# Kernel tuning notes

Measured on AMD Instinct MI355X. Metric: run time of the kernel, lower is better.

The kernel has to match this reference:

```python
import jax, jax.numpy as jnp
import numpy as np

B, T, D_MODEL = 2, 2048, 2048
N_HEAD, N_KV = 16, 4
HEAD_DIM = D_MODEL // N_HEAD  # 128
N_REP = N_HEAD // N_KV        # 4
ROPE_BASE = 10000.0


def setup_inputs() -> dict:
    key = jax.random.key(0)
    ks = jax.random.split(key, 5)
    s = 0.02
    return {
        "x": jax.random.normal(ks[0], (B, T, D_MODEL), dtype=jnp.float32),
        "Wq": jax.random.normal(ks[1], (D_MODEL, N_HEAD * HEAD_DIM), dtype=jnp.float32) * s,
        "Wk": jax.random.normal(ks[2], (D_MODEL, N_KV * HEAD_DIM), dtype=jnp.float32) * s,
        "Wv": jax.random.normal(ks[3], (D_MODEL, N_KV * HEAD_DIM), dtype=jnp.float32) * s,
        "Wo": jax.random.normal(ks[4], (D_MODEL, D_MODEL), dtype=jnp.float32) * s,
    }


def _rope_cos_sin(seq_len, dim, dtype):
    inv_freq = 1.0 / (ROPE_BASE ** (jnp.arange(0, dim, 2, dtype=jnp.float32) / dim))
    t = jnp.arange(seq_len, dtype=jnp.float32)
    freqs = t[:, None] * inv_freq[None, :]          # (T, dim/2)
    emb = jnp.concatenate([freqs, freqs], axis=-1)  # (T, dim)
    return jnp.cos(emb).astype(dtype), jnp.sin(emb).astype(dtype)


def _rotate_half(x):
    half = x.shape[-1] // 2
    return jnp.concatenate([-x[..., half:], x[..., :half]], axis=-1)


def reference(x, Wq, Wk, Wv, Wo):
    Bx, Tx, _ = x.shape
    # projections (weights stored (in, out); equals torch Linear with W^T)
    q = (x @ Wq).reshape(Bx, Tx, N_HEAD, HEAD_DIM).transpose(0, 2, 1, 3)  # (B,H,T,d)
    k = (x @ Wk).reshape(Bx, Tx, N_KV, HEAD_DIM).transpose(0, 2, 1, 3)    # (B,Hkv,T,d)
    v = (x @ Wv).reshape(Bx, Tx, N_KV, HEAD_DIM).transpose(0, 2, 1, 3)

    cos, sin = _rope_cos_sin(Tx, HEAD_DIM, x.dtype)  # (T, d)
    q = q * cos + _rotate_half(q) * sin
    k = k * cos + _rotate_half(k) * sin

    # grouped attention: q grouped by kv head, avoids materializing repeated K/V
    qg = q.reshape(Bx, N_KV, N_REP, Tx, HEAD_DIM)
    scale = 1.0 / np.sqrt(HEAD_DIM)
    att = jnp.einsum('bgrtd,bgsd->bgrts', qg, k) * scale  # (B,Hkv,rep,T,S)
    causal = jnp.tril(jnp.ones((Tx, Tx), dtype=bool))
    att = jnp.where(causal, att, -jnp.inf)
    att = jax.nn.softmax(att, axis=-1)
    y = jnp.einsum('bgrts,bgsd->bgrtd', att, v)           # (B,Hkv,rep,T,d)
    y = y.reshape(Bx, N_HEAD, Tx, HEAD_DIM).transpose(0, 2, 1, 3).reshape(Bx, Tx, D_MODEL)
    return y @ Wo
```

## Files before the change

### kernel.cpp

```cpp
#include <hip/hip_runtime.h>
#include <hip/hip_bf16.h>

typedef unsigned short u16;
typedef unsigned int u32;
typedef __attribute__((ext_vector_type(4))) float f32x4;
typedef __attribute__((ext_vector_type(8))) __bf16 bf16x8;

#define B_   2
#define T_   2048
#define DM   2048
#define NH   16
#define NKV  4
#define HD   128

__device__ __forceinline__ u16 f2bf(float f){
    u32 u = __builtin_bit_cast(u32, f);
    u += 0x7FFFu + ((u >> 16) & 1u);
    return (u16)(u >> 16);
}
__device__ __forceinline__ float bf2f(u16 v){
    return __builtin_bit_cast(float, (u32)v << 16);
}

__device__ __forceinline__ float ex2(float x){
    float r; asm("v_exp_f32 %0, %1" : "=v"(r) : "v"(x)); return r;
}

__device__ __forceinline__ void gld_lds16(const void* g, void* l){
    __builtin_amdgcn_global_load_lds(
        (const __attribute__((address_space(1))) void*)g,
        (__attribute__((address_space(3))) void*)l, 16, 0, 0);
}

__global__ void prep(const float* __restrict__ x,
                     const float* __restrict__ Wq, const float* __restrict__ Wk,
                     const float* __restrict__ Wv, const float* __restrict__ Wo,
                     u16* __restrict__ xb, u16* __restrict__ Wqkv, u16* __restrict__ Wot,
                     float2* __restrict__ tab){
    __shared__ float tile[32][33];
    int bid = blockIdx.x, tid = threadIdx.x;
    if (bid < 8192){
        int i = bid * 256 + tid;
        float4 v = ((const float4*)x)[i];
        ushort4 o;
        o.x = f2bf(v.x); o.y = f2bf(v.y); o.z = f2bf(v.z); o.w = f2bf(v.w);
        ((ushort4*)xb)[i] = o;
    } else if (bid < 18432){
        int tb = bid - 8192;
        int bx = tb % 160, byy = tb / 160;
        const float* W; u16* Out; int N; int nb; int perm;
        if (bx < 64)      { W = Wq; Out = Wqkv;                  N = 2048; nb = bx;      perm = 1; }
        else if (bx < 80) { W = Wk; Out = Wqkv + 2048ull * 2048; N = 512;  nb = bx - 64; perm = 1; }
        else if (bx < 96) { W = Wv; Out = Wqkv + 2560ull * 2048; N = 512;  nb = bx - 80; perm = 0; }
        else              { W = Wo; Out = Wot;                   N = 2048; nb = bx - 96; perm = 0; }
        int n0 = nb * 32, k0 = byy * 32;
        int tx = tid & 31, ty = tid >> 5;
#pragma unroll
        for (int i = 0; i < 4; i++)
            tile[ty + i * 8][tx] = W[(size_t)(k0 + ty + i * 8) * N + n0 + tx];
        __syncthreads();
#pragma unroll
        for (int i = 0; i < 4; i++){
            int n = n0 + ty + i * 8;
            int np = perm ? ((n & ~127) | ((n & 63) << 1) | ((n >> 6) & 1)) : n;
            Out[(size_t)np * 2048 + k0 + tx] = f2bf(tile[tx][ty + i * 8]);
        }
    } else {
        int idx = (bid - 18432) * 256 + tid;
        int i = idx & 63, t = idx >> 6;
        float ang = (float)t * exp2f((float)i * (-13.287712379549449f / 64.0f));
        float sv, cv;
        __sincosf(ang, &sv, &cv);
        tab[idx] = make_float2(cv, sv);
    }
}

#define BARR() asm volatile("s_barrier" ::: "memory")
#define VM4()  asm volatile("s_waitcnt vmcnt(4)" ::: "memory")
#define VM8()  asm volatile("s_waitcnt vmcnt(8)" ::: "memory")

#define READ_A(QA, BUF) { \
    const char* ab = (const char*)&As[BUF][wm][0]; \
    _Pragma("unroll") for (int i = 0; i < 4; i++){ \
        int rh = ((QA)*4 + i)*16 + lx; \
        _Pragma("unroll") for (int ks = 0; ks < 2; ks++) \
            a_[i][ks] = *(const bf16x8*)(ab + rh*128 + (((ks*4+tg)*16) ^ ((lx&7)<<4))); \
    } }
#define READ_B(QB, BUF) { \
    const char* bb = (const char*)&Bs[BUF][wn>>1][0]; \
    _Pragma("unroll") for (int n = 0; n < 2; n++){ \
        int rbh = (wn&1)*64 + ((QB)*2+n)*16 + lx; \
        _Pragma("unroll") for (int ks = 0; ks < 2; ks++) \
            b_[(QB)*2+n][ks] = *(const bf16x8*)(bb + rbh*128 + (((ks*4+tg)*16) ^ ((lx&7)<<4))); \
    } }
#define MFMA_Q(QA, QB) { \
    __builtin_amdgcn_s_setprio(1); \
    _Pragma("unroll") for (int i = 0; i < 4; i++) \
    _Pragma("unroll") for (int n = 0; n < 2; n++) \
    _Pragma("unroll") for (int ks = 0; ks < 2; ks++) \
        acc[(QA)*4+i][(QB)*2+n] = __builtin_amdgcn_mfma_f32_16x16x32_bf16( \
            a_[i][ks], b_[(QB)*2+n][ks], acc[(QA)*4+i][(QB)*2+n], 0, 0, 0); \
    __builtin_amdgcn_s_setprio(0); }

template<int MODE>
__global__ __launch_bounds__(512, 2) void gemm256(const u16* __restrict__ A, const u16* __restrict__ Bt,
                                                  void* __restrict__ O0, u16* __restrict__ Ktl,
                                                  u16* __restrict__ Vtl, const float2* __restrict__ tab,
                                                  int NBX){
    __shared__ __attribute__((aligned(16))) u16 As[2][2][8192];
    __shared__ __attribute__((aligned(16))) u16 Bs[2][2][8192];
    const int tid = threadIdx.x;
    const int lane = tid & 63, w = tid >> 6;
    const int wm = w >> 2, wn = w & 3;
    const int tg = lane >> 4, lx = lane & 15;
    int q8 = (int)gridDim.x >> 3;
    int swz = ((int)blockIdx.x & 7) * q8 + ((int)blockIdx.x >> 3);
    int kh = 0;
    if constexpr (MODE == 2){ kh = swz >> 7; swz &= 127; }
    const int bx = swz % NBX, by = swz / NBX;
    const int m0 = by * 256, n0 = bx * 256;
    const int K = 2048;
    const int NIT = (MODE == 2) ? 8 : 16;
    const int kt0 = kh * 16;
    const int ltMax = 2 * NIT - 1;
    const int kcx = (lane & 7) ^ ((lane >> 3) & 7);

    f32x4 acc[8][4];
    const f32x4 Z = {0.f, 0.f, 0.f, 0.f};
#pragma unroll
    for (int i = 0; i < 8; i++)
#pragma unroll
        for (int j = 0; j < 4; j++) acc[i][j] = Z;
    bf16x8 a_[4][2], b_[4][2];

    auto stA = [&](int buf, int q, int kt){
        int mh = w >> 2;
        int s0 = (w & 3) * 2;
#pragma unroll
        for (int l = 0; l < 2; l++){
            int s = s0 + l;
            gld_lds16(A + (size_t)(m0 + mh*128 + q*64 + s*8 + (lane>>3)) * K + kt*64 + kcx*8,
                      &As[buf][mh][q*4096 + s*512 + lane*8]);
        }
    };
    auto stB = [&](int buf, int q, int kt){
        int bh = w >> 2;
        int hi = (w >> 1) & 1;
        int s0 = (w & 1) * 2;
#pragma unroll
        for (int l = 0; l < 2; l++){
            int s = s0 + l;
            gld_lds16(Bt + (size_t)(n0 + bh*128 + hi*64 + q*32 + s*8 + (lane>>3)) * K + kt*64 + kcx*8,
                      &Bs[buf][bh][hi*4096 + q*2048 + s*512 + lane*8]);
        }
    };

    stA(0, 0, kt0); stB(0, 0, kt0); stA(0, 1, kt0); stB(0, 1, kt0);
    stA(1, 0, kt0 + 1); stB(1, 0, kt0 + 1);
    VM4(); BARR();

#pragma unroll 1
    for (int it = 0; it < NIT; it++){
        const int T1 = kt0 + 2*it + 1;
        const int T2 = kt0 + ((2*it + 2 < ltMax) ? 2*it + 2 : ltMax);
        const int T3 = kt0 + ((2*it + 3 < ltMax) ? 2*it + 3 : ltMax);
        READ_A(0, 0); READ_B(0, 0); stA(1, 1, T1);
        BARR(); MFMA_Q(0, 0); BARR();
        READ_B(1, 0); stB(1, 1, T1);
        BARR(); MFMA_Q(0, 1); BARR();
        READ_A(1, 0); stA(0, 0, T2);
        BARR(); MFMA_Q(1, 0); BARR();
        stB(0, 0, T2);
        BARR(); MFMA_Q(1, 1); VM4(); BARR();
        READ_A(0, 1); READ_B(0, 1); stA(0, 1, T2);
        BARR(); MFMA_Q(0, 0); BARR();
        READ_B(1, 1); stB(0, 1, T2);
        BARR(); MFMA_Q(0, 1); BARR();
        READ_A(1, 1); stA(1, 0, T3);
        BARR(); MFMA_Q(1, 0); BARR();
        stB(1, 0, T3);
        BARR(); MFMA_Q(1, 1); VM4(); BARR();
    }

    if constexpr (MODE == 2){
        u16* C = (u16*)O0 + (size_t)kh * 4096 * 2048;
#pragma unroll
        for (int mi = 0; mi < 8; mi++)
#pragma unroll
            for (int ni = 0; ni < 4; ni++){
                int r0 = m0 + wm*128 + mi*16 + tg*4;
                int c  = n0 + wn*64 + ni*16 + lx;
#pragma unroll
                for (int j = 0; j < 4; j++)
                    C[(size_t)(r0 + j) * 2048 + c] = f2bf(acc[mi][ni][j]);
            }
    } else {
        u16* Qp = (u16*)O0;
        if (bx < 8){
            const float QS = 0.08838834764831845f * 1.4426950408889634f;
#pragma unroll
            for (int mi = 0; mi < 8; mi++)
#pragma unroll
                for (int ni = 0; ni < 4; ni++){
                    int r0 = m0 + wm*128 + mi*16 + tg*4;
                    int c  = n0 + wn*64 + ni*16 + lx;
                    int ii = (c & 127) >> 1;
#pragma unroll
                    for (int j = 0; j < 4; j++){
                        float v = acc[mi][ni][j];
                        float p = __shfl_xor(v, 1);
                        int t = (r0 + j) & 2047;
                        float2 cs = tab[t * 64 + ii];
                        float o = ((lx & 1) ? (v * cs.x + p * cs.y) : (v * cs.x - p * cs.y)) * QS;
                        Qp[(size_t)(r0 + j) * 2048 + c] = f2bf(o);
                    }
                }
        } else if (bx < 10){
#pragma unroll
            for (int mi = 0; mi < 8; mi++)
#pragma unroll
                for (int ni = 0; ni < 4; ni++){
                    int r0 = m0 + wm*128 + mi*16 + tg*4;
                    int c  = n0 + wn*64 + ni*16 + lx;
                    int hk = (c >> 7) & 3;
                    int dd = c & 127;
                    int ii = dd >> 1;
#pragma unroll
                    for (int j = 0; j < 4; j++){
                        int r = r0 + j;
                        int bb2 = r >> 11, tt = r & 2047;
                        float v = acc[mi][ni][j];
                        float p = __shfl_xor(v, 1);
                        float2 cs = tab[tt * 64 + ii];
                        float o = (lx & 1) ? (v * cs.x + p * cs.y) : (v * cs.x - p * cs.y);
                        size_t tb = ((size_t)(bb2 * 4 + hk) * 32 + (tt >> 6)) * 8192;
                        u32 byte = (u32)((tt & 63) * 256) + (((u32)(2 * dd)) ^ ((u32)((tt & 7) << 4)));
                        Ktl[tb + byte / 2] = f2bf(o);
                    }
                }
        } else {
#pragma unroll
            for (int mi = 0; mi < 8; mi++){
                int r0 = m0 + wm*128 + mi*16 + tg*4;
                int bb2 = r0 >> 11, ss = r0 & 2047;
                int sb = ss & 63;
#pragma unroll
                for (int ni = 0; ni < 4; ni++){
                    int c  = n0 + wn*64 + ni*16 + lx;
                    int hk = (c >> 7) & 3;
                    int d  = c & 127;
                    size_t tb = ((size_t)(bb2 * 4 + hk) * 32 + (ss >> 6)) * 8192;
                    u32 swzd = (u32)((d & 7) << 4);
#pragma unroll
                    for (int j = 0; j < 4; j++){
                        int s = sb + j;
                        int sig = ((s & 15) << 2) | ((s >> 4) & 3);
                        u32 byte = (u32)(d * 128) + (((u32)(2 * sig)) ^ swzd);
                        Vtl[tb + byte / 2] = f2bf(acc[mi][ni][j]);
                    }
                }
            }
        }
    }
}

__global__ void reduceWo(const u16* __restrict__ P, float* __restrict__ out){
    size_t t = (size_t)blockIdx.x * 256 + threadIdx.x;
    const u16* p0 = P + t * 8;
    const u16* p1 = P + 4096ull * 2048 + t * 8;
    uint4 a = *(const uint4*)p0;
    uint4 b = *(const uint4*)p1;
    const u16* as = (const u16*)&a;
    const u16* bs = (const u16*)&b;
    float4 o0, o1;
    o0.x = bf2f(as[0]) + bf2f(bs[0]); o0.y = bf2f(as[1]) + bf2f(bs[1]);
    o0.z = bf2f(as[2]) + bf2f(bs[2]); o0.w = bf2f(as[3]) + bf2f(bs[3]);
    o1.x = bf2f(as[4]) + bf2f(bs[4]); o1.y = bf2f(as[5]) + bf2f(bs[5]);
    o1.z = bf2f(as[6]) + bf2f(bs[6]); o1.w = bf2f(as[7]) + bf2f(bs[7]);
    ((float4*)out)[t * 2]     = o0;
    ((float4*)out)[t * 2 + 1] = o1;
}

__global__ __launch_bounds__(256) void attn5(const u16* __restrict__ Q, const u16* __restrict__ Kt,
                                             const u16* __restrict__ Vt, u16* __restrict__ Y){
    __shared__ __attribute__((aligned(16))) u16 Ks[2][64 * 128];
    __shared__ __attribute__((aligned(16))) u16 Vs[2][64 * 128];
    __shared__ __attribute__((aligned(16))) u16 Pl[4][16 * 64];
    const int lane = threadIdx.x & 63, w = threadIdx.x >> 6;
    const int jb = blockIdx.x, h = blockIdx.y, b = blockIdx.z;
    const int hkv = h >> 2;
    const size_t kvBase = ((size_t)(b * NKV + hkv) * 32) * 8192;
    const f32x4 Z = {0.f, 0.f, 0.f, 0.f};
    const int tg = lane >> 4, lx = lane & 15;

    auto STAGE = [&](int buf, int it){
        const u16* kg = Kt + kvBase + (size_t)it * 8192;
        const u16* vg = Vt + kvBase + (size_t)it * 8192;
#pragma unroll
        for (int i = 0; i < 4; i++){
            int is = w * 4 + i;
            gld_lds16(kg + is * 512 + lane * 8, &Ks[buf][is * 512]);
            gld_lds16(vg + is * 512 + lane * 8, &Vs[buf][is * 512]);
        }
    };

#pragma unroll 1
    for (int pass = 0; pass < 2; pass++){
        const int qt = pass == 0 ? jb : 31 - jb;
        const int q0 = qt * 64;
        const int qrow = q0 + w * 16 + lx;
        bf16x8 qfr[4];
#pragma unroll
        for (int kk = 0; kk < 4; kk++)
            qfr[kk] = *(const bf16x8*)(Q + (size_t)(b * T_ + qrow) * DM + h * HD + kk * 32 + tg * 8);
        f32x4 accO[8];
#pragma unroll
        for (int i = 0; i < 8; i++) accO[i] = Z;
        float mr[4] = {-INFINITY, -INFINITY, -INFINITY, -INFINITY};
        float lp[4] = {0.f, 0.f, 0.f, 0.f};
        const int nIter = qt + 1;

        STAGE(0, 0);
        __syncthreads();
        int cur = 0;

#pragma unroll 1
        for (int it = 0; it < nIter; it++){
            if (it + 1 < nIter) STAGE(cur ^ 1, it + 1);
            f32x4 sa[4];
#pragma unroll
            for (int c = 0; c < 4; c++) sa[c] = Z;
            __builtin_amdgcn_s_setprio(1);
#pragma unroll
            for (int c = 0; c < 4; c++){
                int s = c * 16 + lx;
                u32 swz = (u32)((s & 7) << 4);
                const char* kb = (const char*)&Ks[cur][0] + s * 256;
#pragma unroll
                for (int kk = 0; kk < 4; kk++){
                    bf16x8 kf = *(const bf16x8*)(kb + (((u32)(kk * 64 + tg * 16)) ^ swz));
                    sa[c] = __builtin_amdgcn_mfma_f32_16x16x32_bf16(qfr[kk], kf, sa[c], 0, 0, 0);
                }
            }
            __builtin_amdgcn_s_setprio(0);
            const bool diag = (it == nIter - 1);
            float tl[4];
#pragma unroll
            for (int j = 0; j < 4; j++){
                float a0 = sa[0][j], a1 = sa[1][j], a2 = sa[2][j], a3 = sa[3][j];
                if (diag){
                    int qloc = w * 16 + tg * 4 + j;
                    if (lx      > qloc) a0 = -INFINITY;
                    if (lx + 16 > qloc) a1 = -INFINITY;
                    if (lx + 32 > qloc) a2 = -INFINITY;
                    if (lx + 48 > qloc) a3 = -INFINITY;
                }
                sa[0][j] = a0; sa[1][j] = a1; sa[2][j] = a2; sa[3][j] = a3;
                tl[j] = fmaxf(fmaxf(a0, a1), fmaxf(a2, a3));
            }
            int lok = (tl[0] <= mr[0] + 8.f) && (tl[1] <= mr[1] + 8.f) &&
                      (tl[2] <= mr[2] + 8.f) && (tl[3] <= mr[3] + 8.f);
            if (!__all(lok)){
                float corr[4];
#pragma unroll
                for (int j = 0; j < 4; j++){
                    float t = tl[j];
                    t = fmaxf(t, __shfl_xor(t, 1));
                    t = fmaxf(t, __shfl_xor(t, 2));
                    t = fmaxf(t, __shfl_xor(t, 4));
                    t = fmaxf(t, __shfl_xor(t, 8));
                    float mn = fmaxf(mr[j], t);
                    corr[j] = ex2(mr[j] - mn);
                    mr[j] = mn;
                    lp[j] *= corr[j];
                }
#pragma unroll
                for (int dt = 0; dt < 8; dt++){
                    f32x4 t = accO[dt];
                    t[0] *= corr[0]; t[1] *= corr[1]; t[2] *= corr[2]; t[3] *= corr[3];
                    accO[dt] = t;
                }
            }
#pragma unroll
            for (int j = 0; j < 4; j++){
                float mn = mr[j];
                float p0 = ex2(sa[0][j] - mn), p1 = ex2(sa[1][j] - mn);
                float p2 = ex2(sa[2][j] - mn), p3 = ex2(sa[3][j] - mn);
                lp[j] += p0 + p1 + p2 + p3;
                int rr = tg * 4 + j;
                u32 woff = (u32)(rr * 128) + (((u32)(lx * 8)) ^ ((u32)((rr & 7) << 4)));
                u32 r01, r23;
                asm("v_cvt_pk_bf16_f32 %0, %1, %2" : "=v"(r01) : "v"(p0), "v"(p1));
                asm("v_cvt_pk_bf16_f32 %0, %1, %2" : "=v"(r23) : "v"(p2), "v"(p3));
                uint2 pk2 = make_uint2(r01, r23);
                *(uint2*)((char*)&Pl[w][0] + woff) = pk2;
            }
            bf16x8 pf[2];
            {
                char* pb = (char*)&Pl[w][0] + lx * 128;
                u32 swz = (u32)((lx & 7) << 4);
                pf[0] = *(const bf16x8*)(pb + (((u32)(tg * 16))      ^ swz));
                pf[1] = *(const bf16x8*)(pb + (((u32)(tg * 16 + 64)) ^ swz));
            }
            __builtin_amdgcn_s_setprio(1);
#pragma unroll
            for (int dt = 0; dt < 8; dt++){
                int d = dt * 16 + lx;
                u32 swz = (u32)((d & 7) << 4);
                const char* vb = (const char*)&Vs[cur][0] + d * 128;
                bf16x8 vf0 = *(const bf16x8*)(vb + (((u32)(tg * 16))      ^ swz));
                bf16x8 vf1 = *(const bf16x8*)(vb + (((u32)(tg * 16 + 64)) ^ swz));
                accO[dt] = __builtin_amdgcn_mfma_f32_16x16x32_bf16(pf[0], vf0, accO[dt], 0, 0, 0);
                accO[dt] = __builtin_amdgcn_mfma_f32_16x16x32_bf16(pf[1], vf1, accO[dt], 0, 0, 0);
            }
            __builtin_amdgcn_s_setprio(0);
            __syncthreads();
            cur ^= 1;
        }
        float inv[4];
#pragma unroll
        for (int j = 0; j < 4; j++){
            float s = lp[j];
            s += __shfl_xor(s, 1);
            s += __shfl_xor(s, 2);
            s += __shfl_xor(s, 4);
            s += __shfl_xor(s, 8);
            inv[j] = 1.0f / s;
        }
#pragma unroll
        for (int dt = 0; dt < 8; dt++)
#pragma unroll
            for (int j = 0; j < 4; j++){
                int qr = q0 + w * 16 + tg * 4 + j;
                int d = dt * 16 + lx;
                Y[(size_t)(b * T_ + qr) * DM + h * HD + d] = f2bf(accO[dt][j] * inv[j]);
            }
    }
}

extern "C" void kernel_launch(void* const* d_in, const int* in_sizes, int n_in,
                              void* d_out, int out_size, void* d_ws, size_t ws_size,
                              hipStream_t stream){
    const float* x  = (const float*)d_in[0];
    const float* Wq = (const float*)d_in[1];
    const float* Wk = (const float*)d_in[2];
    const float* Wv = (const float*)d_in[3];
    const float* Wo = (const float*)d_in[4];

    char* ws = (char*)d_ws;
    size_t off = 0;
    auto alloc = [&](size_t bytes){ void* p = ws + off; off += (bytes + 255) & ~255ull; return p; };
    u16*    xb   = (u16*)alloc(4096ull * 2048 * 2);
    u16*    Wqkv = (u16*)alloc(3072ull * 2048 * 2);
    u16*    Wot  = (u16*)alloc(2048ull * 2048 * 2);
    u16*    qbb  = (u16*)alloc(4096ull * 2048 * 2);
    u16*    ktl  = (u16*)alloc(2ull * 4 * 32 * 8192 * 2);
    u16*    vtl  = (u16*)alloc(2ull * 4 * 32 * 8192 * 2);
    u16*    ybb  = (u16*)alloc(4096ull * 2048 * 2);
    u16*    pbb  = (u16*)alloc(2ull * 4096 * 2048 * 2);
    float2* tab  = (float2*)alloc(2048ull * 64 * 8);

    prep<<<18944, 256, 0, stream>>>(x, Wq, Wk, Wv, Wo, xb, Wqkv, Wot, tab);

    gemm256<1><<<192, 512, 0, stream>>>(xb, Wqkv, qbb, ktl, vtl, tab, 12);

    attn5<<<dim3(16, 16, 2), 256, 0, stream>>>(qbb, ktl, vtl, ybb);

    gemm256<2><<<256, 512, 0, stream>>>(ybb, Wot, pbb, nullptr, nullptr, nullptr, 8);
    reduceWo<<<4096, 256, 0, stream>>>(pbb, (float*)d_out);
}
```

Baseline: 203.5 us.

## Split attention into single-tile blocks with 32-key tiles and deepen GEMM prefetch

The attention kernel now launches one block per 64-row query tile, 1024 blocks in total, instead of one block looping over two paired tiles. An interleaved block ordering balances the causal workload across blocks. K/V tiles shrink from 64 to 32 keys, and the V layout written by the QKV GEMM epilogue is changed to match, which lowers LDS use and register pressure and should raise occupancy. The price is more loop iterations and barriers per block. The GEMM main loop also issues the whole next k-tile earlier and waits with vmcnt(8), aiming to hide more global-load latency.

New measurement: 225.9 us. +11.0%, slower.

```diff
diff --git a/kernel.cpp b/kernel.cpp
--- a/kernel.cpp
+++ b/kernel.cpp
@@ -76,7 +76,6 @@
 }
 
 #define BARR() asm volatile("s_barrier" ::: "memory")
-#define VM4()  asm volatile("s_waitcnt vmcnt(4)" ::: "memory")
 #define VM8()  asm volatile("s_waitcnt vmcnt(8)" ::: "memory")
 
 #define READ_A(QA, BUF) { \
@@ -156,30 +155,29 @@
     };
 
     stA(0, 0, kt0); stB(0, 0, kt0); stA(0, 1, kt0); stB(0, 1, kt0);
-    stA(1, 0, kt0 + 1); stB(1, 0, kt0 + 1);
-    VM4(); BARR();
+    stA(1, 0, kt0 + 1); stB(1, 0, kt0 + 1); stB(1, 1, kt0 + 1); stA(1, 1, kt0 + 1);
+    VM8(); BARR();
 
 #pragma unroll 1
     for (int it = 0; it < NIT; it++){
-        const int T1 = kt0 + 2*it + 1;
         const int T2 = kt0 + ((2*it + 2 < ltMax) ? 2*it + 2 : ltMax);
         const int T3 = kt0 + ((2*it + 3 < ltMax) ? 2*it + 3 : ltMax);
-        READ_A(0, 0); READ_B(0, 0); stA(1, 1, T1);
+        READ_A(0, 0); READ_B(0, 0);
         BARR(); MFMA_Q(0, 0); BARR();
-        READ_B(1, 0); stB(1, 1, T1);
+        READ_B(1, 0); stA(0, 0, T2); stB(0, 0, T2);
         BARR(); MFMA_Q(0, 1); BARR();
-        READ_A(1, 0); stA(0, 0, T2);
+        READ_A(1, 0); stB(0, 1, T2);
         BARR(); MFMA_Q(1, 0); BARR();
-        stB(0, 0, T2);
-        BARR(); MFMA_Q(1, 1); VM4(); BARR();
-        READ_A(0, 1); READ_B(0, 1); stA(0, 1, T2);
+        stA(0, 1, T2);
+        BARR(); MFMA_Q(1, 1); VM8(); BARR();
+        READ_A(0, 1); READ_B(0, 1);
         BARR(); MFMA_Q(0, 0); BARR();
-        READ_B(1, 1); stB(0, 1, T2);
+        READ_B(1, 1); stA(1, 0, T3); stB(1, 0, T3);
         BARR(); MFMA_Q(0, 1); BARR();
-        READ_A(1, 1); stA(1, 0, T3);
+        READ_A(1, 1); stB(1, 1, T3);
         BARR(); MFMA_Q(1, 0); BARR();
-        stB(1, 0, T3);
-        BARR(); MFMA_Q(1, 1); VM4(); BARR();
+        stA(1, 1, T3);
+        BARR(); MFMA_Q(1, 1); VM8(); BARR();
     }
 
     if constexpr (MODE == 2){
@@ -243,20 +241,20 @@
             for (int mi = 0; mi < 8; mi++){
                 int r0 = m0 + wm*128 + mi*16 + tg*4;
                 int bb2 = r0 >> 11, ss = r0 & 2047;
-                int sb = ss & 63;
+                int sb = ss & 31;
 #pragma unroll
                 for (int ni = 0; ni < 4; ni++){
                     int c  = n0 + wn*64 + ni*16 + lx;
                     int hk = (c >> 7) & 3;
                     int d  = c & 127;
-                    size_t tb = ((size_t)(bb2 * 4 + hk) * 32 + (ss >> 6)) * 8192;
-                    u32 swzd = (u32)((d & 7) << 4);
+                    size_t tbh = ((size_t)(bb2 * 4 + hk) * 64 + (ss >> 5)) * 4096;
+                    u32 swzd = (u32)((d & 3) << 4);
 #pragma unroll
                     for (int j = 0; j < 4; j++){
                         int s = sb + j;
-                        int sig = ((s & 15) << 2) | ((s >> 4) & 3);
-                        u32 byte = (u32)(d * 128) + (((u32)(2 * sig)) ^ swzd);
-                        Vtl[tb + byte / 2] = f2bf(acc[mi][ni][j]);
+                        int sig = ((s & 15) << 1) | ((s >> 4) & 1);
+                        u32 byte = (u32)(d * 64) + (((u32)(2 * sig)) ^ swzd);
+                        Vtl[tbh + byte / 2] = f2bf(acc[mi][ni][j]);
                     }
                 }
             }
@@ -281,161 +279,149 @@
     ((float4*)out)[t * 2 + 1] = o1;
 }
 
-__global__ __launch_bounds__(256) void attn5(const u16* __restrict__ Q, const u16* __restrict__ Kt,
+__global__ __launch_bounds__(256) void attn7(const u16* __restrict__ Q, const u16* __restrict__ Kt,
                                              const u16* __restrict__ Vt, u16* __restrict__ Y){
-    __shared__ __attribute__((aligned(16))) u16 Ks[2][64 * 128];
-    __shared__ __attribute__((aligned(16))) u16 Vs[2][64 * 128];
-    __shared__ __attribute__((aligned(16))) u16 Pl[4][16 * 64];
-    const int lane = threadIdx.x & 63, w = threadIdx.x >> 6;
-    const int jb = blockIdx.x, h = blockIdx.y, b = blockIdx.z;
+    __shared__ __attribute__((aligned(16))) u16 Ks[2][4096];
+    __shared__ __attribute__((aligned(16))) u16 Vs[2][4096];
+    __shared__ __attribute__((aligned(16))) u16 Pl[4][512];
+    const int tid = threadIdx.x;
+    const int lane = tid & 63, w = tid >> 6;
+    const int tg = lane >> 4, lx = lane & 15;
+    int gid = blockIdx.x;
+    int z = gid & 255, k4 = gid >> 8;
+    int j8 = z & 7, h = (z >> 3) & 15, b = z >> 7;
+    int qt = (k4 == 0) ? j8 : (k4 == 1) ? 31 - j8 : (k4 == 2) ? j8 + 8 : 23 - j8;
     const int hkv = h >> 2;
-    const size_t kvBase = ((size_t)(b * NKV + hkv) * 32) * 8192;
+    const size_t kvBase = (size_t)(b * NKV + hkv) * 64 * 4096;
     const f32x4 Z = {0.f, 0.f, 0.f, 0.f};
-    const int tg = lane >> 4, lx = lane & 15;
 
     auto STAGE = [&](int buf, int it){
-        const u16* kg = Kt + kvBase + (size_t)it * 8192;
-        const u16* vg = Vt + kvBase + (size_t)it * 8192;
-#pragma unroll
-        for (int i = 0; i < 4; i++){
-            int is = w * 4 + i;
-            gld_lds16(kg + is * 512 + lane * 8, &Ks[buf][is * 512]);
-            gld_lds16(vg + is * 512 + lane * 8, &Vs[buf][is * 512]);
-        }
+        const u16* kg = Kt + kvBase + (size_t)it * 4096;
+        const u16* vg = Vt + kvBase + (size_t)it * 4096;
+        gld_lds16(kg + tid * 8,        &Ks[buf][tid * 8]);
+        gld_lds16(kg + 2048 + tid * 8, &Ks[buf][2048 + tid * 8]);
+        gld_lds16(vg + tid * 8,        &Vs[buf][tid * 8]);
+        gld_lds16(vg + 2048 + tid * 8, &Vs[buf][2048 + tid * 8]);
     };
 
+    const int q0 = qt * 64;
+    const int qrow = q0 + w * 16 + lx;
+    bf16x8 qfr[4];
+#pragma unroll
+    for (int kk = 0; kk < 4; kk++)
+        qfr[kk] = *(const bf16x8*)(Q + (size_t)(b * T_ + qrow) * DM + h * HD + kk * 32 + tg * 8);
+    f32x4 accO[8];
+#pragma unroll
+    for (int i = 0; i < 8; i++) accO[i] = Z;
+    float mr[4] = {-INFINITY, -INFINITY, -INFINITY, -INFINITY};
+    float lp[4] = {0.f, 0.f, 0.f, 0.f};
+    const int nIter = 2 * qt + 2;
+
+    STAGE(0, 0);
+    __syncthreads();
+    int cur = 0;
+
 #pragma unroll 1
-    for (int pass = 0; pass < 2; pass++){
-        const int qt = pass == 0 ? jb : 31 - jb;
-        const int q0 = qt * 64;
-        const int qrow = q0 + w * 16 + lx;
-        bf16x8 qfr[4];
-#pragma unroll
-        for (int kk = 0; kk < 4; kk++)
-            qfr[kk] = *(const bf16x8*)(Q + (size_t)(b * T_ + qrow) * DM + h * HD + kk * 32 + tg * 8);
-        f32x4 accO[8];
-#pragma unroll
-        for (int i = 0; i < 8; i++) accO[i] = Z;
-        float mr[4] = {-INFINITY, -INFINITY, -INFINITY, -INFINITY};
-        float lp[4] = {0.f, 0.f, 0.f, 0.f};
-        const int nIter = qt + 1;
-
-        STAGE(0, 0);
+    for (int it = 0; it < nIter; it++){
+        if (it + 1 < nIter) STAGE(cur ^ 1, it + 1);
+        f32x4 sa[2];
+        sa[0] = Z; sa[1] = Z;
+        __builtin_amdgcn_s_setprio(1);
+#pragma unroll
+        for (int c = 0; c < 2; c++){
+            int s = c * 16 + lx;
+            u32 swz = (u32)((s & 7) << 4);
+            const char* kb = (const char*)&Ks[cur][0] + s * 256;
+#pragma unroll
+            for (int kk = 0; kk < 4; kk++){
+                bf16x8 kf = *(const bf16x8*)(kb + (((u32)(kk * 64 + tg * 16)) ^ swz));
+                sa[c] = __builtin_amdgcn_mfma_f32_16x16x32_bf16(qfr[kk], kf, sa[c], 0, 0, 0);
+            }
+        }
+        __builtin_amdgcn_s_setprio(0);
+        const int s0g = it * 32;
+        const bool diag = (s0g + 31 > q0 + w * 16);
+        float tl[4];
+#pragma unroll
+        for (int j = 0; j < 4; j++){
+            float a0 = sa[0][j], a1 = sa[1][j];
+            if (diag){
+                int qg = q0 + w * 16 + tg * 4 + j;
+                if (s0g + lx > qg)      a0 = -INFINITY;
+                if (s0g + 16 + lx > qg) a1 = -INFINITY;
+            }
+            sa[0][j] = a0; sa[1][j] = a1;
+            tl[j] = fmaxf(a0, a1);
+        }
+        int lok = (tl[0] <= mr[0] + 8.f) && (tl[1] <= mr[1] + 8.f) &&
+                  (tl[2] <= mr[2] + 8.f) && (tl[3] <= mr[3] + 8.f);
+        if (!__all(lok)){
+            float corr[4];
+#pragma unroll
+            for (int j = 0; j < 4; j++){
+                float t = tl[j];
+                t = fmaxf(t, __shfl_xor(t, 1));
+                t = fmaxf(t, __shfl_xor(t, 2));
+                t = fmaxf(t, __shfl_xor(t, 4));
+                t = fmaxf(t, __shfl_xor(t, 8));
+                float mn = fmaxf(mr[j], t);
+                corr[j] = ex2(mr[j] - mn);
+                mr[j] = mn;
+                lp[j] *= corr[j];
+            }
+#pragma unroll
+            for (int dt = 0; dt < 8; dt++){
+                f32x4 t = accO[dt];
+                t[0] *= corr[0]; t[1] *= corr[1]; t[2] *= corr[2]; t[3] *= corr[3];
+                accO[dt] = t;
+            }
+        }
+#pragma unroll
+        for (int j = 0; j < 4; j++){
+            float mn = mr[j];
+            float p0 = ex2(sa[0][j] - mn), p1 = ex2(sa[1][j] - mn);
+            lp[j] += p0 + p1;
+            int rr = tg * 4 + j;
+            u32 woff = (u32)(rr * 64) + (((u32)(lx * 4)) ^ ((u32)((rr & 3) << 4)));
+            u32 r01;
+            asm("v_cvt_pk_bf16_f32 %0, %1, %2" : "=v"(r01) : "v"(p0), "v"(p1));
+            *(u32*)((char*)&Pl[w][0] + woff) = r01;
+        }
+        bf16x8 pf;
+        {
+            char* pb = (char*)&Pl[w][0] + lx * 64;
+            pf = *(const bf16x8*)(pb + (((u32)(tg * 16)) ^ ((u32)((lx & 3) << 4))));
+        }
+        __builtin_amdgcn_s_setprio(1);
+#pragma unroll
+        for (int dt = 0; dt < 8; dt++){
+            int d = dt * 16 + lx;
+            const char* vb = (const char*)&Vs[cur][0] + d * 64;
+            bf16x8 vf = *(const bf16x8*)(vb + (((u32)(tg * 16)) ^ ((u32)((d & 3) << 4))));
+            accO[dt] = __builtin_amdgcn_mfma_f32_16x16x32_bf16(pf, vf, accO[dt], 0, 0, 0);
+        }
+        __builtin_amdgcn_s_setprio(0);
         __syncthreads();
-        int cur = 0;
-
-#pragma unroll 1
-        for (int it = 0; it < nIter; it++){
-            if (it + 1 < nIter) STAGE(cur ^ 1, it + 1);
-            f32x4 sa[4];
-#pragma unroll
-            for (int c = 0; c < 4; c++) sa[c] = Z;
-            __builtin_amdgcn_s_setprio(1);
-#pragma unroll
-            for (int c = 0; c < 4; c++){
-                int s = c * 16 + lx;
-                u32 swz = (u32)((s & 7) << 4);
-                const char* kb = (const char*)&Ks[cur][0] + s * 256;
-#pragma unroll
-                for (int kk = 0; kk < 4; kk++){
-                    bf16x8 kf = *(const bf16x8*)(kb + (((u32)(kk * 64 + tg * 16)) ^ swz));
-                    sa[c] = __builtin_amdgcn_mfma_f32_16x16x32_bf16(qfr[kk], kf, sa[c], 0, 0, 0);
-                }
-            }
-            __builtin_amdgcn_s_setprio(0);
-            const bool diag = (it == nIter - 1);
-            float tl[4];
-#pragma unroll
-            for (int j = 0; j < 4; j++){
-                float a0 = sa[0][j], a1 = sa[1][j], a2 = sa[2][j], a3 = sa[3][j];
-                if (diag){
-                    int qloc = w * 16 + tg * 4 + j;
-                    if (lx      > qloc) a0 = -INFINITY;
-                    if (lx + 16 > qloc) a1 = -INFINITY;
-                    if (lx + 32 > qloc) a2 = -INFINITY;
-                    if (lx + 48 > qloc) a3 = -INFINITY;
-                }
-                sa[0][j] = a0; sa[1][j] = a1; sa[2][j] = a2; sa[3][j] = a3;
-                tl[j] = fmaxf(fmaxf(a0, a1), fmaxf(a2, a3));
-            }
-            int lok = (tl[0] <= mr[0] + 8.f) && (tl[1] <= mr[1] + 8.f) &&
-                      (tl[2] <= mr[2] + 8.f) && (tl[3] <= mr[3] + 8.f);
-            if (!__all(lok)){
-                float corr[4];
-#pragma unroll
-                for (int j = 0; j < 4; j++){
-                    float t = tl[j];
-                    t = fmaxf(t, __shfl_xor(t, 1));
-                    t = fmaxf(t, __shfl_xor(t, 2));
-                    t = fmaxf(t, __shfl_xor(t, 4));
-                    t = fmaxf(t, __shfl_xor(t, 8));
-                    float mn = fmaxf(mr[j], t);
-                    corr[j] = ex2(mr[j] - mn);
-                    mr[j] = mn;
-                    lp[j] *= corr[j];
-                }
-#pragma unroll
-                for (int dt = 0; dt < 8; dt++){
-                    f32x4 t = accO[dt];
-                    t[0] *= corr[0]; t[1] *= corr[1]; t[2] *= corr[2]; t[3] *= corr[3];
-                    accO[dt] = t;
-                }
-            }
-#pragma unroll
-            for (int j = 0; j < 4; j++){
-                float mn = mr[j];
-                float p0 = ex2(sa[0][j] - mn), p1 = ex2(sa[1][j] - mn);
-                float p2 = ex2(sa[2][j] - mn), p3 = ex2(sa[3][j] - mn);
-                lp[j] += p0 + p1 + p2 + p3;
-                int rr = tg * 4 + j;
-                u32 woff = (u32)(rr * 128) + (((u32)(lx * 8)) ^ ((u32)((rr & 7) << 4)));
-                u32 r01, r23;
-                asm("v_cvt_pk_bf16_f32 %0, %1, %2" : "=v"(r01) : "v"(p0), "v"(p1));
-                asm("v_cvt_pk_bf16_f32 %0, %1, %2" : "=v"(r23) : "v"(p2), "v"(p3));
-                uint2 pk2 = make_uint2(r01, r23);
-                *(uint2*)((char*)&Pl[w][0] + woff) = pk2;
-            }
-            bf16x8 pf[2];
-            {
-                char* pb = (char*)&Pl[w][0] + lx * 128;
-                u32 swz = (u32)((lx & 7) << 4);
-                pf[0] = *(const bf16x8*)(pb + (((u32)(tg * 16))      ^ swz));
-                pf[1] = *(const bf16x8*)(pb + (((u32)(tg * 16 + 64)) ^ swz));
-            }
-            __builtin_amdgcn_s_setprio(1);
-#pragma unroll
-            for (int dt = 0; dt < 8; dt++){
-                int d = dt * 16 + lx;
-                u32 swz = (u32)((d & 7) << 4);
-                const char* vb = (const char*)&Vs[cur][0] + d * 128;
-                bf16x8 vf0 = *(const bf16x8*)(vb + (((u32)(tg * 16))      ^ swz));
-                bf16x8 vf1 = *(const bf16x8*)(vb + (((u32)(tg * 16 + 64)) ^ swz));
-                accO[dt] = __builtin_amdgcn_mfma_f32_16x16x32_bf16(pf[0], vf0, accO[dt], 0, 0, 0);
-                accO[dt] = __builtin_amdgcn_mfma_f32_16x16x32_bf16(pf[1], vf1, accO[dt], 0, 0, 0);
-            }
-            __builtin_amdgcn_s_setprio(0);
-            __syncthreads();
-            cur ^= 1;
-        }
-        float inv[4];
+        cur ^= 1;
+    }
+    float inv[4];
+#pragma unroll
+    for (int j = 0; j < 4; j++){
+        float s = lp[j];
+        s += __shfl_xor(s, 1);
+        s += __shfl_xor(s, 2);
+        s += __shfl_xor(s, 4);
+        s += __shfl_xor(s, 8);
+        inv[j] = 1.0f / s;
+    }
+#pragma unroll
+    for (int dt = 0; dt < 8; dt++)
 #pragma unroll
         for (int j = 0; j < 4; j++){
-            float s = lp[j];
-            s += __shfl_xor(s, 1);
-            s += __shfl_xor(s, 2);
-            s += __shfl_xor(s, 4);
-            s += __shfl_xor(s, 8);
-            inv[j] = 1.0f / s;
-        }
-#pragma unroll
-        for (int dt = 0; dt < 8; dt++)
-#pragma unroll
-            for (int j = 0; j < 4; j++){
-                int qr = q0 + w * 16 + tg * 4 + j;
-                int d = dt * 16 + lx;
-                Y[(size_t)(b * T_ + qr) * DM + h * HD + d] = f2bf(accO[dt][j] * inv[j]);
-            }
-    }
+            int qr = q0 + w * 16 + tg * 4 + j;
+            int d = dt * 16 + lx;
+            Y[(size_t)(b * T_ + qr) * DM + h * HD + d] = f2bf(accO[dt][j] * inv[j]);
+        }
 }
 
 extern "C" void kernel_launch(void* const* d_in, const int* in_sizes, int n_in,
@@ -454,8 +440,8 @@
     u16*    Wqkv = (u16*)alloc(3072ull * 2048 * 2);
     u16*    Wot  = (u16*)alloc(2048ull * 2048 * 2);
     u16*    qbb  = (u16*)alloc(4096ull * 2048 * 2);
-    u16*    ktl  = (u16*)alloc(2ull * 4 * 32 * 8192 * 2);
-    u16*    vtl  = (u16*)alloc(2ull * 4 * 32 * 8192 * 2);
+    u16*    ktl  = (u16*)alloc(2ull * 4 * 64 * 4096 * 2);
+    u16*    vtl  = (u16*)alloc(2ull * 4 * 64 * 4096 * 2);
     u16*    ybb  = (u16*)alloc(4096ull * 2048 * 2);
     u16*    pbb  = (u16*)alloc(2ull * 4096 * 2048 * 2);
     float2* tab  = (float2*)alloc(2048ull * 64 * 8);
@@ -464,7 +450,7 @@
 
     gemm256<1><<<192, 512, 0, stream>>>(xb, Wqkv, qbb, ktl, vtl, tab, 12);
 
-    attn5<<<dim3(16, 16, 2), 256, 0, stream>>>(qbb, ktl, vtl, ybb);
+    attn7<<<1024, 256, 0, stream>>>(qbb, ktl, vtl, ybb);
 
     gemm256<2><<<256, 512, 0, stream>>>(ybb, Wot, pbb, nullptr, nullptr, nullptr, 8);
     reduceWo<<<4096, 256, 0, stream>>>(pbb, (float*)d_out);
```

## Split attention into one q-tile per block with single-buffered K/V staggered prefetch

Applied to the files above, without the earlier changes.

The attention kernel now launches 1024 blocks that each handle one 64-row query tile, where before 512 blocks each ran two causal-balanced passes. Work is ordered so that long and short tiles interleave across the launch. K and V each use a single LDS buffer instead of a double buffer. The next K tile is loaded while softmax and PV run, and the next V tile is loaded after PV, with explicit vmcnt waits and barriers. This halves LDS use so more blocks can be resident and latency is hidden across blocks, at the cost of extra barriers and less prefetch distance within a block.

After: 202.1 us. Within noise of the previous version (-0.7%).

```diff
diff --git a/kernel.cpp b/kernel.cpp
--- a/kernel.cpp
+++ b/kernel.cpp
@@ -76,8 +76,8 @@
 }
 
 #define BARR() asm volatile("s_barrier" ::: "memory")
+#define VM0()  asm volatile("s_waitcnt vmcnt(0)" ::: "memory")
 #define VM4()  asm volatile("s_waitcnt vmcnt(4)" ::: "memory")
-#define VM8()  asm volatile("s_waitcnt vmcnt(8)" ::: "memory")
 
 #define READ_A(QA, BUF) { \
     const char* ab = (const char*)&As[BUF][wm][0]; \
@@ -281,161 +281,170 @@
     ((float4*)out)[t * 2 + 1] = o1;
 }
 
-__global__ __launch_bounds__(256) void attn5(const u16* __restrict__ Q, const u16* __restrict__ Kt,
+__global__ __launch_bounds__(256) void attn8(const u16* __restrict__ Q, const u16* __restrict__ Kt,
                                              const u16* __restrict__ Vt, u16* __restrict__ Y){
-    __shared__ __attribute__((aligned(16))) u16 Ks[2][64 * 128];
-    __shared__ __attribute__((aligned(16))) u16 Vs[2][64 * 128];
-    __shared__ __attribute__((aligned(16))) u16 Pl[4][16 * 64];
-    const int lane = threadIdx.x & 63, w = threadIdx.x >> 6;
-    const int jb = blockIdx.x, h = blockIdx.y, b = blockIdx.z;
+    __shared__ __attribute__((aligned(16))) u16 Ks[8192];
+    __shared__ __attribute__((aligned(16))) u16 Vs[8192];
+    __shared__ __attribute__((aligned(16))) u16 Pl[4][1024];
+    const int tid = threadIdx.x;
+    const int lane = tid & 63, w = tid >> 6;
+    const int tg = lane >> 4, lx = lane & 15;
+    int gid = blockIdx.x;
+    int z = gid & 255, k4 = gid >> 8;
+    int j8 = z & 7, h = (z >> 3) & 15, b = z >> 7;
+    int qt = (k4 == 0) ? j8 : (k4 == 1) ? 31 - j8 : (k4 == 2) ? j8 + 8 : 23 - j8;
     const int hkv = h >> 2;
     const size_t kvBase = ((size_t)(b * NKV + hkv) * 32) * 8192;
     const f32x4 Z = {0.f, 0.f, 0.f, 0.f};
-    const int tg = lane >> 4, lx = lane & 15;
-
-    auto STAGE = [&](int buf, int it){
+
+    auto STAGE_K = [&](int it){
         const u16* kg = Kt + kvBase + (size_t)it * 8192;
-        const u16* vg = Vt + kvBase + (size_t)it * 8192;
 #pragma unroll
         for (int i = 0; i < 4; i++){
             int is = w * 4 + i;
-            gld_lds16(kg + is * 512 + lane * 8, &Ks[buf][is * 512]);
-            gld_lds16(vg + is * 512 + lane * 8, &Vs[buf][is * 512]);
+            gld_lds16(kg + is * 512 + lane * 8, &Ks[is * 512]);
         }
     };
+    auto STAGE_V = [&](int it){
+        const u16* vg = Vt + kvBase + (size_t)it * 8192;
+#pragma unroll
+        for (int i = 0; i < 4; i++){
+            int is = w * 4 + i;
+            gld_lds16(vg + is * 512 + lane * 8, &Vs[is * 512]);
+        }
+    };
+
+    const int q0 = qt * 64;
+    const int qrow = q0 + w * 16 + lx;
+    bf16x8 qfr[4];
+#pragma unroll
+    for (int kk = 0; kk < 4; kk++)
+        qfr[kk] = *(const bf16x8*)(Q + (size_t)(b * T_ + qrow) * DM + h * HD + kk * 32 + tg * 8);
+    f32x4 accO[8];
+#pragma unroll
+    for (int i = 0; i < 8; i++) accO[i] = Z;
+    float mr[4] = {-INFINITY, -INFINITY, -INFINITY, -INFINITY};
+    float lp[4] = {0.f, 0.f, 0.f, 0.f};
+    const int nIter = qt + 1;
+
+    STAGE_K(0); STAGE_V(0);
 
 #pragma unroll 1
-    for (int pass = 0; pass < 2; pass++){
-        const int qt = pass == 0 ? jb : 31 - jb;
-        const int q0 = qt * 64;
-        const int qrow = q0 + w * 16 + lx;
-        bf16x8 qfr[4];
-#pragma unroll
-        for (int kk = 0; kk < 4; kk++)
-            qfr[kk] = *(const bf16x8*)(Q + (size_t)(b * T_ + qrow) * DM + h * HD + kk * 32 + tg * 8);
-        f32x4 accO[8];
-#pragma unroll
-        for (int i = 0; i < 8; i++) accO[i] = Z;
-        float mr[4] = {-INFINITY, -INFINITY, -INFINITY, -INFINITY};
-        float lp[4] = {0.f, 0.f, 0.f, 0.f};
-        const int nIter = qt + 1;
-
-        STAGE(0, 0);
-        __syncthreads();
-        int cur = 0;
-
-#pragma unroll 1
-        for (int it = 0; it < nIter; it++){
-            if (it + 1 < nIter) STAGE(cur ^ 1, it + 1);
-            f32x4 sa[4];
-#pragma unroll
-            for (int c = 0; c < 4; c++) sa[c] = Z;
-            __builtin_amdgcn_s_setprio(1);
-#pragma unroll
-            for (int c = 0; c < 4; c++){
-                int s = c * 16 + lx;
-                u32 swz = (u32)((s & 7) << 4);
-                const char* kb = (const char*)&Ks[cur][0] + s * 256;
-#pragma unroll
-                for (int kk = 0; kk < 4; kk++){
-                    bf16x8 kf = *(const bf16x8*)(kb + (((u32)(kk * 64 + tg * 16)) ^ swz));
-                    sa[c] = __builtin_amdgcn_mfma_f32_16x16x32_bf16(qfr[kk], kf, sa[c], 0, 0, 0);
-                }
-            }
-            __builtin_amdgcn_s_setprio(0);
-            const bool diag = (it == nIter - 1);
-            float tl[4];
+    for (int it = 0; it < nIter; it++){
+        const bool last = (it + 1 == nIter);
+        VM4(); BARR();
+        f32x4 sa[4];
+#pragma unroll
+        for (int c = 0; c < 4; c++) sa[c] = Z;
+        __builtin_amdgcn_s_setprio(1);
+#pragma unroll
+        for (int c = 0; c < 4; c++){
+            int s = c * 16 + lx;
+            u32 swz = (u32)((s & 7) << 4);
+            const char* kb = (const char*)&Ks[0] + s * 256;
+#pragma unroll
+            for (int kk = 0; kk < 4; kk++){
+                bf16x8 kf = *(const bf16x8*)(kb + (((u32)(kk * 64 + tg * 16)) ^ swz));
+                sa[c] = __builtin_amdgcn_mfma_f32_16x16x32_bf16(qfr[kk], kf, sa[c], 0, 0, 0);
+            }
+        }
+        __builtin_amdgcn_s_setprio(0);
+        BARR();
+        if (!last) STAGE_K(it + 1);
+        const bool diag = last;
+        float tl[4];
+#pragma unroll
+        for (int j = 0; j < 4; j++){
+            float a0 = sa[0][j], a1 = sa[1][j], a2 = sa[2][j], a3 = sa[3][j];
+            if (diag){
+                int qloc = w * 16 + tg * 4 + j;
+                if (lx      > qloc) a0 = -INFINITY;
+                if (lx + 16 > qloc) a1 = -INFINITY;
+                if (lx + 32 > qloc) a2 = -INFINITY;
+                if (lx + 48 > qloc) a3 = -INFINITY;
+            }
+            sa[0][j] = a0; sa[1][j] = a1; sa[2][j] = a2; sa[3][j] = a3;
+            tl[j] = fmaxf(fmaxf(a0, a1), fmaxf(a2, a3));
+        }
+        int lok = (tl[0] <= mr[0] + 8.f) && (tl[1] <= mr[1] + 8.f) &&
+                  (tl[2] <= mr[2] + 8.f) && (tl[3] <= mr[3] + 8.f);
+        if (!__all(lok)){
+            float corr[4];
 #pragma unroll
             for (int j = 0; j < 4; j++){
-                float a0 = sa[0][j], a1 = sa[1][j], a2 = sa[2][j], a3 = sa[3][j];
-                if (diag){
-                    int qloc = w * 16 + tg * 4 + j;
-                    if (lx      > qloc) a0 = -INFINITY;
-                    if (lx + 16 > qloc) a1 = -INFINITY;
-                    if (lx + 32 > qloc) a2 = -INFINITY;
-                    if (lx + 48 > qloc) a3 = -INFINITY;
-                }
-                sa[0][j] = a0; sa[1][j] = a1; sa[2][j] = a2; sa[3][j] = a3;
-                tl[j] = fmaxf(fmaxf(a0, a1), fmaxf(a2, a3));
-            }
-            int lok = (tl[0] <= mr[0] + 8.f) && (tl[1] <= mr[1] + 8.f) &&
-                      (tl[2] <= mr[2] + 8.f) && (tl[3] <= mr[3] + 8.f);
-            if (!__all(lok)){
-                float corr[4];
-#pragma unroll
-                for (int j = 0; j < 4; j++){
-                    float t = tl[j];
-                    t = fmaxf(t, __shfl_xor(t, 1));
-                    t = fmaxf(t, __shfl_xor(t, 2));
-                    t = fmaxf(t, __shfl_xor(t, 4));
-                    t = fmaxf(t, __shfl_xor(t, 8));
-                    float mn = fmaxf(mr[j], t);
-                    corr[j] = ex2(mr[j] - mn);
-                    mr[j] = mn;
-                    lp[j] *= corr[j];
-                }
-#pragma unroll
-                for (int dt = 0; dt < 8; dt++){
-                    f32x4 t = accO[dt];
-                    t[0] *= corr[0]; t[1] *= corr[1]; t[2] *= corr[2]; t[3] *= corr[3];
-                    accO[dt] = t;
-                }
-            }
-#pragma unroll
-            for (int j = 0; j < 4; j++){
-                float mn = mr[j];
-                float p0 = ex2(sa[0][j] - mn), p1 = ex2(sa[1][j] - mn);
-                float p2 = ex2(sa[2][j] - mn), p3 = ex2(sa[3][j] - mn);
-                lp[j] += p0 + p1 + p2 + p3;
-                int rr = tg * 4 + j;
-                u32 woff = (u32)(rr * 128) + (((u32)(lx * 8)) ^ ((u32)((rr & 7) << 4)));
-                u32 r01, r23;
-                asm("v_cvt_pk_bf16_f32 %0, %1, %2" : "=v"(r01) : "v"(p0), "v"(p1));
-                asm("v_cvt_pk_bf16_f32 %0, %1, %2" : "=v"(r23) : "v"(p2), "v"(p3));
-                uint2 pk2 = make_uint2(r01, r23);
-                *(uint2*)((char*)&Pl[w][0] + woff) = pk2;
-            }
-            bf16x8 pf[2];
-            {
-                char* pb = (char*)&Pl[w][0] + lx * 128;
-                u32 swz = (u32)((lx & 7) << 4);
-                pf[0] = *(const bf16x8*)(pb + (((u32)(tg * 16))      ^ swz));
-                pf[1] = *(const bf16x8*)(pb + (((u32)(tg * 16 + 64)) ^ swz));
-            }
-            __builtin_amdgcn_s_setprio(1);
+                float t = tl[j];
+                t = fmaxf(t, __shfl_xor(t, 1));
+                t = fmaxf(t, __shfl_xor(t, 2));
+                t = fmaxf(t, __shfl_xor(t, 4));
+                t = fmaxf(t, __shfl_xor(t, 8));
+                float mn = fmaxf(mr[j], t);
+                corr[j] = ex2(mr[j] - mn);
+                mr[j] = mn;
+                lp[j] *= corr[j];
+            }
 #pragma unroll
             for (int dt = 0; dt < 8; dt++){
-                int d = dt * 16 + lx;
-                u32 swz = (u32)((d & 7) << 4);
-                const char* vb = (const char*)&Vs[cur][0] + d * 128;
-                bf16x8 vf0 = *(const bf16x8*)(vb + (((u32)(tg * 16))      ^ swz));
-                bf16x8 vf1 = *(const bf16x8*)(vb + (((u32)(tg * 16 + 64)) ^ swz));
-                accO[dt] = __builtin_amdgcn_mfma_f32_16x16x32_bf16(pf[0], vf0, accO[dt], 0, 0, 0);
-                accO[dt] = __builtin_amdgcn_mfma_f32_16x16x32_bf16(pf[1], vf1, accO[dt], 0, 0, 0);
-            }
-            __builtin_amdgcn_s_setprio(0);
-            __syncthreads();
-            cur ^= 1;
-        }
-        float inv[4];
+                f32x4 t = accO[dt];
+                t[0] *= corr[0]; t[1] *= corr[1]; t[2] *= corr[2]; t[3] *= corr[3];
+                accO[dt] = t;
+            }
+        }
 #pragma unroll
         for (int j = 0; j < 4; j++){
-            float s = lp[j];
-            s += __shfl_xor(s, 1);
-            s += __shfl_xor(s, 2);
-            s += __shfl_xor(s, 4);
-            s += __shfl_xor(s, 8);
-            inv[j] = 1.0f / s;
-        }
-#pragma unroll
-        for (int dt = 0; dt < 8; dt++)
-#pragma unroll
-            for (int j = 0; j < 4; j++){
-                int qr = q0 + w * 16 + tg * 4 + j;
-                int d = dt * 16 + lx;
-                Y[(size_t)(b * T_ + qr) * DM + h * HD + d] = f2bf(accO[dt][j] * inv[j]);
-            }
+            float mn = mr[j];
+            float p0 = ex2(sa[0][j] - mn), p1 = ex2(sa[1][j] - mn);
+            float p2 = ex2(sa[2][j] - mn), p3 = ex2(sa[3][j] - mn);
+            lp[j] += p0 + p1 + p2 + p3;
+            int rr = tg * 4 + j;
+            u32 woff = (u32)(rr * 128) + (((u32)(lx * 8)) ^ ((u32)((rr & 7) << 4)));
+            u32 r01, r23;
+            asm("v_cvt_pk_bf16_f32 %0, %1, %2" : "=v"(r01) : "v"(p0), "v"(p1));
+            asm("v_cvt_pk_bf16_f32 %0, %1, %2" : "=v"(r23) : "v"(p2), "v"(p3));
+            uint2 pk2 = make_uint2(r01, r23);
+            *(uint2*)((char*)&Pl[w][0] + woff) = pk2;
+        }
+        bf16x8 pf[2];
+        {
+            char* pb = (char*)&Pl[w][0] + lx * 128;
+            u32 swz = (u32)((lx & 7) << 4);
+            pf[0] = *(const bf16x8*)(pb + (((u32)(tg * 16))      ^ swz));
+            pf[1] = *(const bf16x8*)(pb + (((u32)(tg * 16 + 64)) ^ swz));
+        }
+        if (last){ VM0(); } else { VM4(); }
+        BARR();
+        __builtin_amdgcn_s_setprio(1);
+#pragma unroll
+        for (int dt = 0; dt < 8; dt++){
+            int d = dt * 16 + lx;
+            u32 swz = (u32)((d & 7) << 4);
+            const char* vb = (const char*)&Vs[0] + d * 128;
+            bf16x8 vf0 = *(const bf16x8*)(vb + (((u32)(tg * 16))      ^ swz));
+            bf16x8 vf1 = *(const bf16x8*)(vb + (((u32)(tg * 16 + 64)) ^ swz));
+            accO[dt] = __builtin_amdgcn_mfma_f32_16x16x32_bf16(pf[0], vf0, accO[dt], 0, 0, 0);
+            accO[dt] = __builtin_amdgcn_mfma_f32_16x16x32_bf16(pf[1], vf1, accO[dt], 0, 0, 0);
+        }
+        __builtin_amdgcn_s_setprio(0);
+        BARR();
+        if (!last) STAGE_V(it + 1);
     }
+    float inv[4];
+#pragma unroll
+    for (int j = 0; j < 4; j++){
+        float s = lp[j];
+        s += __shfl_xor(s, 1);
+        s += __shfl_xor(s, 2);
+        s += __shfl_xor(s, 4);
+        s += __shfl_xor(s, 8);
+        inv[j] = 1.0f / s;
+    }
+#pragma unroll
+    for (int dt = 0; dt < 8; dt++)
+#pragma unroll
+        for (int j = 0; j < 4; j++){
+            int qr = q0 + w * 16 + tg * 4 + j;
+            int d = dt * 16 + lx;
+            Y[(size_t)(b * T_ + qr) * DM + h * HD + d] = f2bf(accO[dt][j] * inv[j]);
+        }
 }
 
 extern "C" void kernel_launch(void* const* d_in, const int* in_sizes, int n_in,
@@ -464,7 +473,7 @@
 
     gemm256<1><<<192, 512, 0, stream>>>(xb, Wqkv, qbb, ktl, vtl, tab, 12);
 
-    attn5<<<dim3(16, 16, 2), 256, 0, stream>>>(qbb, ktl, vtl, ybb);
+    attn8<<<1024, 256, 0, stream>>>(qbb, ktl, vtl, ybb);
 
     gemm256<2><<<256, 512, 0, stream>>>(ybb, Wot, pbb, nullptr, nullptr, nullptr, 8);
     reduceWo<<<4096, 256, 0, stream>>>(pbb, (float*)d_out);
```
